# Performance work log

Measured on AMD Instinct MI355X. Metric: run time of the kernel, lower is better.

The kernel has to match this reference:

```python
import jax, jax.numpy as jnp
import numpy as np


def _block(x, W, b, use_relu):
    # x: (B, n, dx). Faithful to PairwiseInteractions: full pairwise L2 dist,
    # top-k (k == n) smallest sorted, drop self, concat(self, neighbor), linear,
    # optional relu, mean over the n-1 neighbors.
    B, n, dx = x.shape
    sq = jnp.sum(x * x, axis=-1)                                   # (B, n)
    d2 = sq[:, :, None] + sq[:, None, :] - 2.0 * jnp.einsum('bnd,bmd->bnm', x, x)
    dist = jnp.sqrt(jnp.maximum(d2, 0.0))                          # (B, n, n)
    _, idx = jax.lax.top_k(-dist, n)                               # ascending distances
    idx_nb = idx[:, :, 1:]                                         # drop self -> (B, n, n-1)
    nbr = jnp.take_along_axis(x[:, None, :, :], idx_nb[..., None], axis=2)  # (B, n, n-1, dx)
    self_rep = jnp.broadcast_to(x[:, :, None, :], nbr.shape)
    pairs = jnp.concatenate([self_rep, nbr], axis=-1)              # (B, n, n-1, 2*dx)
    h = pairs @ W + b
    if use_relu:
        h = jax.nn.relu(h)
    return jnp.sum(h, axis=2) / (n - 1)                            # (B, n, d_out)


def setup_inputs() -> dict:
    key = jax.random.key(0)
    ks = jax.random.split(key, 4)
    B, N, d = 2, 1024, 3

    def lin(k, fin, fout):
        kw, kb = jax.random.split(k)
        lim = 1.0 / np.sqrt(fin).astype(np.float32)
        W = jax.random.uniform(kw, (fin, fout), minval=-lim, maxval=lim, dtype=jnp.float32)
        b = jax.random.uniform(kb, (fout,), minval=-lim, maxval=lim, dtype=jnp.float32)
        return W, b

    W1, b1 = lin(ks[1], 2 * d, 32)
    W2, b2 = lin(ks[2], 2 * 32, 64)
    W3, b3 = lin(ks[3], 2 * 64, d)
    x = jax.random.normal(ks[0], (B, N * d), dtype=jnp.float32)
    return {"x": x, "W1": W1, "b1": b1, "W2": W2, "b2": b2, "W3": W3, "b3": b3}


def reference(x, W1, b1, W2, b2, W3, b3):
    B = x.shape[0]
    d = W3.shape[1]
    N = x.shape[1] // d
    h = x.reshape(B, N, d)
    h = _block(h, W1, b1, True)    # eb1: d -> 32, relu
    h = _block(h, W2, b2, True)    # eb2: 32 -> 64, relu
    h = _block(h, W3, b3, False)   # eb3: 64 -> d, no relu
    return h.reshape(B, N * d)
```

## Files before the change

kernel.cpp:

```cpp
#include <hip/hip_runtime.h>

typedef float float2v __attribute__((ext_vector_type(2)));
typedef float float4v __attribute__((ext_vector_type(4)));

#define NN 1024

__global__ __launch_bounds__(256) void k1_pair32_ac2(
    const float* __restrict__ x,  const float* __restrict__ W1, const float* __restrict__ b1,
    const float* __restrict__ W2, const float* __restrict__ b2,
    float* __restrict__ a2g, float* __restrict__ c2g)
{
    __shared__ float xbuf[3072];
    __shared__ float cbuf[8192];
    __shared__ float rowbuf[4][32];

    const int tid  = threadIdx.x;
    const int wave = tid >> 6, lane = tid & 63;
    const int blk  = blockIdx.x;

    const int i  = blk * 4 + wave;
    const int b  = i >> 10;
    const int il = i & 1023;
    const int js = lane >> 4;
    const int fp = lane & 15;

    const float4v* xb4 = (const float4v*)(x + b * 3072);
    {
        float4v* xd = (float4v*)xbuf;
        #pragma unroll
        for (int n = 0; n < 3; ++n) xd[tid + n * 256] = xb4[tid + n * 256];
    }
    __syncthreads();

    const float xi0 = xbuf[il*3+0], xi1 = xbuf[il*3+1], xi2 = xbuf[il*3+2];
    const float2v* W1v = (const float2v*)W1;
    const float2v* b1v = (const float2v*)b1;
    float2v a  = xi0*W1v[0*16+fp] + xi1*W1v[1*16+fp] + xi2*W1v[2*16+fp];
    float2v cs = xi0*W1v[3*16+fp] + xi1*W1v[4*16+fp] + xi2*W1v[5*16+fp] + b1v[fp];

    const int fp2 = tid & 15, r0 = tid >> 4;
    const float2v w3 = W1v[3*16+fp2], w4 = W1v[4*16+fp2], w5 = W1v[5*16+fp2];
    const float2v bb = b1v[fp2];

    float2v acc = (float2v)0.f;
    float2v* cb2w = (float2v*)cbuf;
    const float2v* cb2 = (const float2v*)cbuf;
    for (int tile = 0; tile < NN; tile += 256) {
        #pragma unroll
        for (int k = 0; k < 16; ++k) {
            int r = r0 + k * 16;
            int g = tile + r;
            float y0 = xbuf[g*3+0], y1 = xbuf[g*3+1], y2 = xbuf[g*3+2];
            cb2w[r*16 + fp2] = y0*w3 + y1*w4 + y2*w5 + bb;
        }
        __syncthreads();
        #pragma unroll 8
        for (int k = 0; k < 64; ++k) {
            float2v c = cb2[(4*k + js)*16 + fp];
            acc += __builtin_elementwise_max(a + c, (float2v)0.f);
        }
        __syncthreads();
    }
    acc.x += __shfl_xor(acc.x, 16);  acc.y += __shfl_xor(acc.y, 16);
    acc.x += __shfl_xor(acc.x, 32);  acc.y += __shfl_xor(acc.y, 32);

    float2v self = __builtin_elementwise_max(a + cs, (float2v)0.f);
    float2v res  = (acc - self) * (1.0f/1023.0f);
    if (js == 0) ((float2v*)rowbuf[wave])[fp] = res;
    __syncthreads();

    float av = 0.f, cv = b2[lane];
    #pragma unroll
    for (int d = 0; d < 32; ++d) {
        float hv = rowbuf[wave][d];
        av += hv * W2[d*64 + lane];
        cv += hv * W2[(32 + d)*64 + lane];
    }
    a2g[i*64 + lane] = av;
    c2g[i*64 + lane] = cv;
}

__global__ __launch_bounds__(256) void k2_pair64_final(
    const float* __restrict__ a2g, const float* __restrict__ c2g,
    const float* __restrict__ W3, const float* __restrict__ b3,
    float* __restrict__ out, float* __restrict__ partials)
{
    __shared__ float cbuf[8192];
    __shared__ float2v pacc[4][4][32];
    __shared__ float qpart[4][3];

    const int tid  = threadIdx.x;
    const int wave = tid >> 6, lane = tid & 63;
    const int blk  = blockIdx.x;

    const int i0 = blk * 4;
    const int b  = blk >> 8;
    const int jq = lane >> 5, fp = lane & 31;

    const float* cb = c2g + b * (NN * 64);
    const float2v* a2v = (const float2v*)a2g;
    const float2v a0 = a2v[(i0+0)*32 + fp];
    const float2v a1 = a2v[(i0+1)*32 + fp];
    const float2v a2 = a2v[(i0+2)*32 + fp];
    const float2v a3 = a2v[(i0+3)*32 + fp];
    float2v s0 = (float2v)0.f, s1 = (float2v)0.f, s2 = (float2v)0.f, s3 = (float2v)0.f;

    const float4v* src = (const float4v*)cb;
    const float2v* cb2 = (const float2v*)cbuf;
    const int jbase = 2*wave + jq;
    for (int tile = 0; tile < NN; tile += 128) {
        const float4v* sp = src + tile * 16;
        float4v* dst = (float4v*)cbuf;
        #pragma unroll
        for (int n = 0; n < 8; ++n) dst[tid + n*256] = sp[tid + n*256];
        __syncthreads();
        #pragma unroll
        for (int k = 0; k < 16; ++k) {
            float2v c = cb2[(8*k + jbase)*32 + fp];
            s0 += __builtin_elementwise_max(a0 + c, (float2v)0.f);
            s1 += __builtin_elementwise_max(a1 + c, (float2v)0.f);
            s2 += __builtin_elementwise_max(a2 + c, (float2v)0.f);
            s3 += __builtin_elementwise_max(a3 + c, (float2v)0.f);
        }
        __syncthreads();
    }
    s0.x += __shfl_xor(s0.x, 32);  s0.y += __shfl_xor(s0.y, 32);
    s1.x += __shfl_xor(s1.x, 32);  s1.y += __shfl_xor(s1.y, 32);
    s2.x += __shfl_xor(s2.x, 32);  s2.y += __shfl_xor(s2.y, 32);
    s3.x += __shfl_xor(s3.x, 32);  s3.y += __shfl_xor(s3.y, 32);
    if (jq == 0) {
        pacc[wave][0][fp] = s0;  pacc[wave][1][fp] = s1;
        pacc[wave][2][fp] = s2;  pacc[wave][3][fp] = s3;
    }
    __syncthreads();

    const int i = i0 + wave;
    float2v racc = pacc[0][wave][fp] + pacc[1][wave][fp]
                 + pacc[2][wave][fp] + pacc[3][wave][fp];
    const float2v* cbv = (const float2v*)cb;
    const float inv = 1.0f/1023.0f;
    float2v ai   = a2v[i*32 + fp];
    float2v self = __builtin_elementwise_max(ai + cbv[(i & 1023)*32 + fp], (float2v)0.f);
    float2v res  = (racc - self) * inv;

    float y[3], q[3];
    #pragma unroll
    for (int t = 0; t < 3; ++t) {
        float wt0 = W3[(2*fp)*3 + t],   wb0 = W3[(64 + 2*fp)*3 + t];
        float wt1 = W3[(2*fp+1)*3 + t], wb1 = W3[(64 + 2*fp+1)*3 + t];
        y[t] = res.x*(wt0 - wb0*inv) + res.y*(wt1 - wb1*inv);
        q[t] = res.x*wb0 + res.y*wb1;
    }
    #pragma unroll
    for (int off = 1; off < 32; off <<= 1) {
        #pragma unroll
        for (int t = 0; t < 3; ++t) {
            y[t] += __shfl_xor(y[t], off);
            q[t] += __shfl_xor(q[t], off);
        }
    }
    if (lane == 0) {
        out[i*3+0] = y[0] + b3[0];
        out[i*3+1] = y[1] + b3[1];
        out[i*3+2] = y[2] + b3[2];
        qpart[wave][0] = q[0];  qpart[wave][1] = q[1];  qpart[wave][2] = q[2];
    }
    __syncthreads();
    if (tid < 3)
        partials[blk*3 + tid] = qpart[0][tid] + qpart[1][tid] + qpart[2][tid] + qpart[3][tid];
}

__global__ __launch_bounds__(256) void k3_final(
    const float* __restrict__ partials, float* __restrict__ out)
{
    __shared__ float red[4][3];

    const int tid  = threadIdx.x;
    const int wave = tid >> 6, lane = tid & 63;
    const int blk  = blockIdx.x;
    const int b = blk >> 2;

    const float* pb = partials + b * 256 * 3;
    float s0 = pb[tid*3+0], s1 = pb[tid*3+1], s2 = pb[tid*3+2];
    #pragma unroll
    for (int off = 32; off; off >>= 1) {
        s0 += __shfl_xor(s0, off);  s1 += __shfl_xor(s1, off);  s2 += __shfl_xor(s2, off);
    }
    if (lane == 0) { red[wave][0] = s0; red[wave][1] = s1; red[wave][2] = s2; }
    __syncthreads();
    float S0 = (red[0][0]+red[1][0]+red[2][0]+red[3][0]) * (1.0f/1023.0f);
    float S1 = (red[0][1]+red[1][1]+red[2][1]+red[3][1]) * (1.0f/1023.0f);
    float S2 = (red[0][2]+red[1][2]+red[2][2]+red[3][2]) * (1.0f/1023.0f);

    const int i = b * NN + (blk & 3) * 256 + tid;
    out[i*3+0] += S0;
    out[i*3+1] += S1;
    out[i*3+2] += S2;
}

extern "C" void kernel_launch(void* const* d_in, const int* in_sizes, int n_in,
                              void* d_out, int out_size, void* d_ws, size_t ws_size,
                              hipStream_t stream) {
    const float* x  = (const float*)d_in[0];
    const float* W1 = (const float*)d_in[1];
    const float* b1 = (const float*)d_in[2];
    const float* W2 = (const float*)d_in[3];
    const float* b2 = (const float*)d_in[4];
    const float* W3 = (const float*)d_in[5];
    const float* b3 = (const float*)d_in[6];
    float* out = (float*)d_out;

    float* ws = (float*)d_ws;
    float* a2g      = ws;
    float* c2g      = a2g + 131072;
    float* partials = c2g + 131072;

    k1_pair32_ac2<<<512, 256, 0, stream>>>(x, W1, b1, W2, b2, a2g, c2g);
    k2_pair64_final<<<512, 256, 0, stream>>>(a2g, c2g, W3, b3, out, partials);
    k3_final<<<8, 256, 0, stream>>>(partials, out);
}
```

Before: 104.5 us.

## Fuse final reduction into k2 via grid-wide atomic barrier; read c2g directly from global

Removes the third kernel launch by having the last block of k2 reduce the per-block partials and publish per-batch sums through a flag that every block spin-waits on before writing its output. It also drops the LDS staging of c2g in k2 and reads it straight from global/L2 without block barriers. The spin-wait assumes all 512 blocks are co-resident, otherwise it deadlocks until the iteration cap expires and then reads stale sums. Direct global loads trade LDS traffic and syncs for cache bandwidth.

```diff
diff --git a/kernel.cpp b/kernel.cpp
--- a/kernel.cpp
+++ b/kernel.cpp
@@ -8,7 +8,7 @@
 __global__ __launch_bounds__(256) void k1_pair32_ac2(
     const float* __restrict__ x,  const float* __restrict__ W1, const float* __restrict__ b1,
     const float* __restrict__ W2, const float* __restrict__ b2,
-    float* __restrict__ a2g, float* __restrict__ c2g)
+    float* __restrict__ a2g, float* __restrict__ c2g, unsigned int* __restrict__ syncw)
 {
     __shared__ float xbuf[3072];
     __shared__ float cbuf[8192];
@@ -17,6 +17,7 @@
     const int tid  = threadIdx.x;
     const int wave = tid >> 6, lane = tid & 63;
     const int blk  = blockIdx.x;
+    if (blk == 0 && tid < 8) syncw[tid] = 0u;
 
     const int i  = blk * 4 + wave;
     const int b  = i >> 10;
@@ -83,11 +84,14 @@
 __global__ __launch_bounds__(256) void k2_pair64_final(
     const float* __restrict__ a2g, const float* __restrict__ c2g,
     const float* __restrict__ W3, const float* __restrict__ b3,
-    float* __restrict__ out, float* __restrict__ partials)
+    float* __restrict__ out, float* __restrict__ partials,
+    unsigned int* __restrict__ syncw)
 {
-    __shared__ float cbuf[8192];
     __shared__ float2v pacc[4][4][32];
     __shared__ float qpart[4][3];
+    __shared__ float redbuf[4][6];
+    __shared__ float sS[6];
+    __shared__ unsigned int sLast;
 
     const int tid  = threadIdx.x;
     const int wave = tid >> 6, lane = tid & 63;
@@ -96,8 +100,14 @@
     const int i0 = blk * 4;
     const int b  = blk >> 8;
     const int jq = lane >> 5, fp = lane & 31;
+    const float inv = 1.0f/1023.0f;
+
+    unsigned int* counter = syncw;
+    unsigned int* flag    = syncw + 1;
+    float*        Sg      = (float*)(syncw + 2);
 
     const float* cb = c2g + b * (NN * 64);
+    const float2v* cbv = (const float2v*)cb;
     const float2v* a2v = (const float2v*)a2g;
     const float2v a0 = a2v[(i0+0)*32 + fp];
     const float2v a1 = a2v[(i0+1)*32 + fp];
@@ -105,24 +115,15 @@
     const float2v a3 = a2v[(i0+3)*32 + fp];
     float2v s0 = (float2v)0.f, s1 = (float2v)0.f, s2 = (float2v)0.f, s3 = (float2v)0.f;
 
-    const float4v* src = (const float4v*)cb;
-    const float2v* cb2 = (const float2v*)cbuf;
     const int jbase = 2*wave + jq;
-    for (int tile = 0; tile < NN; tile += 128) {
-        const float4v* sp = src + tile * 16;
-        float4v* dst = (float4v*)cbuf;
-        #pragma unroll
-        for (int n = 0; n < 8; ++n) dst[tid + n*256] = sp[tid + n*256];
-        __syncthreads();
-        #pragma unroll
-        for (int k = 0; k < 16; ++k) {
-            float2v c = cb2[(8*k + jbase)*32 + fp];
-            s0 += __builtin_elementwise_max(a0 + c, (float2v)0.f);
-            s1 += __builtin_elementwise_max(a1 + c, (float2v)0.f);
-            s2 += __builtin_elementwise_max(a2 + c, (float2v)0.f);
-            s3 += __builtin_elementwise_max(a3 + c, (float2v)0.f);
-        }
-        __syncthreads();
+    const float2v* cj = cbv + jbase*32 + fp;
+    #pragma unroll 16
+    for (int k = 0; k < 128; ++k) {
+        float2v c = cj[k * 256];
+        s0 += __builtin_elementwise_max(a0 + c, (float2v)0.f);
+        s1 += __builtin_elementwise_max(a1 + c, (float2v)0.f);
+        s2 += __builtin_elementwise_max(a2 + c, (float2v)0.f);
+        s3 += __builtin_elementwise_max(a3 + c, (float2v)0.f);
     }
     s0.x += __shfl_xor(s0.x, 32);  s0.y += __shfl_xor(s0.y, 32);
     s1.x += __shfl_xor(s1.x, 32);  s1.y += __shfl_xor(s1.y, 32);
@@ -137,8 +138,6 @@
     const int i = i0 + wave;
     float2v racc = pacc[0][wave][fp] + pacc[1][wave][fp]
                  + pacc[2][wave][fp] + pacc[3][wave][fp];
-    const float2v* cbv = (const float2v*)cb;
-    const float inv = 1.0f/1023.0f;
     float2v ai   = a2v[i*32 + fp];
     float2v self = __builtin_elementwise_max(ai + cbv[(i & 1023)*32 + fp], (float2v)0.f);
     float2v res  = (racc - self) * inv;
@@ -159,43 +158,67 @@
             q[t] += __shfl_xor(q[t], off);
         }
     }
+    if (lane == 0) { qpart[wave][0] = q[0]; qpart[wave][1] = q[1]; qpart[wave][2] = q[2]; }
+    __syncthreads();
+
+    if (tid < 3) {
+        float p = qpart[0][tid] + qpart[1][tid] + qpart[2][tid] + qpart[3][tid];
+        __hip_atomic_store(&partials[blk*3 + tid], p, __ATOMIC_RELAXED, __HIP_MEMORY_SCOPE_AGENT);
+    }
+    asm volatile("s_waitcnt vmcnt(0)" ::: "memory");
+    __syncthreads();
+    if (tid == 0) {
+        unsigned int old = __hip_atomic_fetch_add(counter, 1u, __ATOMIC_RELAXED, __HIP_MEMORY_SCOPE_AGENT);
+        sLast = (old == 511u) ? 1u : 0u;
+    }
+    __syncthreads();
+
+    if (sLast) {
+        float p0[3], p1[3];
+        #pragma unroll
+        for (int t = 0; t < 3; ++t) {
+            p0[t] = __hip_atomic_load(&partials[tid*3 + t],        __ATOMIC_RELAXED, __HIP_MEMORY_SCOPE_AGENT);
+            p1[t] = __hip_atomic_load(&partials[(256+tid)*3 + t],  __ATOMIC_RELAXED, __HIP_MEMORY_SCOPE_AGENT);
+        }
+        #pragma unroll
+        for (int off = 1; off < 64; off <<= 1) {
+            #pragma unroll
+            for (int t = 0; t < 3; ++t) {
+                p0[t] += __shfl_xor(p0[t], off);
+                p1[t] += __shfl_xor(p1[t], off);
+            }
+        }
+        if (lane == 0) {
+            #pragma unroll
+            for (int t = 0; t < 3; ++t) { redbuf[wave][t] = p0[t]; redbuf[wave][3+t] = p1[t]; }
+        }
+        __syncthreads();
+        if (tid < 6) {
+            float v = redbuf[0][tid] + redbuf[1][tid] + redbuf[2][tid] + redbuf[3][tid];
+            __hip_atomic_store(&Sg[tid], v, __ATOMIC_RELAXED, __HIP_MEMORY_SCOPE_AGENT);
+        }
+        asm volatile("s_waitcnt vmcnt(0)" ::: "memory");
+        __syncthreads();
+        if (tid == 0)
+            __hip_atomic_store(flag, 1u, __ATOMIC_RELAXED, __HIP_MEMORY_SCOPE_AGENT);
+    }
+
+    if (tid == 0) {
+        int it = 0;
+        while (__hip_atomic_load(flag, __ATOMIC_RELAXED, __HIP_MEMORY_SCOPE_AGENT) == 0u) {
+            __builtin_amdgcn_s_sleep(1);
+            if (++it > (1 << 18)) break;
+        }
+    }
+    __syncthreads();
+    if (tid < 6) sS[tid] = __hip_atomic_load(&Sg[tid], __ATOMIC_RELAXED, __HIP_MEMORY_SCOPE_AGENT);
+    __syncthreads();
+
     if (lane == 0) {
-        out[i*3+0] = y[0] + b3[0];
-        out[i*3+1] = y[1] + b3[1];
-        out[i*3+2] = y[2] + b3[2];
-        qpart[wave][0] = q[0];  qpart[wave][1] = q[1];  qpart[wave][2] = q[2];
-    }
-    __syncthreads();
-    if (tid < 3)
-        partials[blk*3 + tid] = qpart[0][tid] + qpart[1][tid] + qpart[2][tid] + qpart[3][tid];
-}
-
-__global__ __launch_bounds__(256) void k3_final(
-    const float* __restrict__ partials, float* __restrict__ out)
-{
-    __shared__ float red[4][3];
-
-    const int tid  = threadIdx.x;
-    const int wave = tid >> 6, lane = tid & 63;
-    const int blk  = blockIdx.x;
-    const int b = blk >> 2;
-
-    const float* pb = partials + b * 256 * 3;
-    float s0 = pb[tid*3+0], s1 = pb[tid*3+1], s2 = pb[tid*3+2];
-    #pragma unroll
-    for (int off = 32; off; off >>= 1) {
-        s0 += __shfl_xor(s0, off);  s1 += __shfl_xor(s1, off);  s2 += __shfl_xor(s2, off);
-    }
-    if (lane == 0) { red[wave][0] = s0; red[wave][1] = s1; red[wave][2] = s2; }
-    __syncthreads();
-    float S0 = (red[0][0]+red[1][0]+red[2][0]+red[3][0]) * (1.0f/1023.0f);
-    float S1 = (red[0][1]+red[1][1]+red[2][1]+red[3][1]) * (1.0f/1023.0f);
-    float S2 = (red[0][2]+red[1][2]+red[2][2]+red[3][2]) * (1.0f/1023.0f);
-
-    const int i = b * NN + (blk & 3) * 256 + tid;
-    out[i*3+0] += S0;
-    out[i*3+1] += S1;
-    out[i*3+2] += S2;
+        out[i*3+0] = y[0] + b3[0] + sS[b*3+0] * inv;
+        out[i*3+1] = y[1] + b3[1] + sS[b*3+1] * inv;
+        out[i*3+2] = y[2] + b3[2] + sS[b*3+2] * inv;
+    }
 }
 
 extern "C" void kernel_launch(void* const* d_in, const int* in_sizes, int n_in,
@@ -214,8 +237,8 @@
     float* a2g      = ws;
     float* c2g      = a2g + 131072;
     float* partials = c2g + 131072;
-
-    k1_pair32_ac2<<<512, 256, 0, stream>>>(x, W1, b1, W2, b2, a2g, c2g);
-    k2_pair64_final<<<512, 256, 0, stream>>>(a2g, c2g, W3, b3, out, partials);
-    k3_final<<<8, 256, 0, stream>>>(partials, out);
+    unsigned int* syncw = (unsigned int*)(partials + 1536);
+
+    k1_pair32_ac2<<<512, 256, 0, stream>>>(x, W1, b1, W2, b2, a2g, c2g, syncw);
+    k2_pair64_final<<<512, 256, 0, stream>>>(a2g, c2g, W3, b3, out, partials, syncw);
 }
```

After: 117.9 us. +12.8%, slower.
